# Kernel tuning notes

Hardware: AMD Instinct MI355X
Metric: run time of the kernel (lower is better)

Reference implementation:

```python
import jax, jax.numpy as jnp
import numpy as np

N, K, C, OUT = 2048, 14, 512, 512
SCALE = 4.0
BN_EPS = 1e-5


def _edge_lists(k):
    # pairs i<j with i,j != k-1 and adj[i,j] > 0 (adj is fully connected ones)
    ei, ej = [], []
    for i in range(k - 1):
        for j in range(i + 1, k - 1):
            ei.append(i)
            ej.append(j)
    return np.asarray(ei, np.int32), np.asarray(ej, np.int32)


def setup_inputs() -> dict:
    key = jax.random.key(0)
    k0, k1, k2, k3 = jax.random.split(key, 4)
    ei, ej = _edge_lists(K)
    std = 0.02
    return {
        "inputs": jax.random.normal(k0, (N, K, C), dtype=jnp.float32),
        "adj": jnp.ones((K, K), dtype=jnp.float32),
        "edge_i": jnp.asarray(ei),
        "edge_j": jnp.asarray(ej),
        "gamma": jnp.ones((C,), dtype=jnp.float32),
        "beta": jnp.zeros((C,), dtype=jnp.float32),
        "w_direct": jax.random.normal(k1, (C,), dtype=jnp.float32) * std,
        "W_merged": jax.random.normal(k2, (OUT, C), dtype=jnp.float32) * std,
        "W_orig": jax.random.normal(k3, (OUT, C), dtype=jnp.float32) * std,
    }


def reference(inputs, adj, edge_i, edge_j, gamma, beta, w_direct, W_merged, W_orig):
    n, k, c = inputs.shape
    # --- learn_adj ---
    global_feat = inputs[:, k - 1 : k, :]                      # [N,1,c]
    distances = jnp.abs(inputs - global_feat)                  # [N,k,c]
    # pairwise gaps only on the static edge list (i<j, non-global, adj>0)
    gap = 15.0 * (distances[:, edge_i, :] - distances[:, edge_j, :])  # [N,E,c]
    # BatchNorm1d over channel c, batch stats over (N, E), biased variance
    mean = jnp.mean(gap, axis=(0, 1))
    var = jnp.mean(jnp.square(gap - mean), axis=(0, 1))
    bn = (gap - mean) * (gamma / jnp.sqrt(var + BN_EPS)) + beta        # [N,E,c]
    a = jax.nn.sigmoid(SCALE * jnp.einsum("nec,c->ne", bn, w_direct))  # [N,E]
    adj2 = jnp.ones((n, k, k), dtype=inputs.dtype)
    adj2 = adj2.at[:, edge_i, edge_j].set(2.0 * a)
    adj2 = adj2.at[:, edge_j, edge_i].set(2.0 * (1.0 - a))
    new_adj = adj2 * adj[None, :, :]
    norm = jnp.sum(jnp.abs(new_adj), axis=2, keepdims=True)    # L1 row norm
    new_adj = new_adj / jnp.maximum(norm, 1e-12)
    # --- graph conv ---
    agg = jnp.einsum("nij,njc->nic", new_adj, inputs)          # [N,k,c]
    merged = jax.nn.relu(jnp.einsum("nkc,oc->nko", agg, W_merged))
    original = jnp.einsum("nkc,oc->nko", inputs, W_orig)
    return merged + original
```

## Files before the change

kernel.cpp:

```cpp
#include <hip/hip_runtime.h>
#include <stdint.h>

#define K_NODES 14
#define C_DIM   512
#define OUT_DIM 512
#define N_EDGE  78

typedef float  f32x4  __attribute__((ext_vector_type(4)));
typedef __bf16 bf16x8 __attribute__((ext_vector_type(8)));

__device__ __forceinline__ unsigned short f2bf(float f) {
    unsigned int u = __builtin_bit_cast(unsigned int, f);
    unsigned int r = (u + 0x7fffu + ((u >> 16) & 1u)) >> 16;
    return (unsigned short)r;
}
__device__ __forceinline__ float bf2f(unsigned short s) {
    return __builtin_bit_cast(float, (unsigned int)s << 16);
}

__device__ __forceinline__ void async16(const void* g, void* l) {
    __builtin_amdgcn_global_load_lds(
        (const __attribute__((address_space(1))) unsigned int*)g,
        (__attribute__((address_space(3))) unsigned int*)l, 16, 0, 0);
}

__global__ __launch_bounds__(1024) void stats_partial(
    const float* __restrict__ x, float* __restrict__ part,
    unsigned short* __restrict__ xbf,
    const float* __restrict__ Wm, const float* __restrict__ Wo,
    unsigned short* __restrict__ wmbf, unsigned short* __restrict__ wobf)
{
    int t  = threadIdx.x;
    int q  = t & 127;
    int sn = t >> 7;
    int n  = blockIdx.x * 8 + sn;
    size_t base = (size_t)n * K_NODES * C_DIM + q * 4;

    f32x4 g = *(const f32x4*)(x + base + 13 * C_DIM);
    ushort4 gb; gb.x=f2bf(g.x); gb.y=f2bf(g.y); gb.z=f2bf(g.z); gb.w=f2bf(g.w);
    *(ushort4*)(xbf + base + 13 * C_DIM) = gb;

    float S10=0,S11=0,S12=0,S13=0, S20=0,S21=0,S22=0,S23=0, Sw0=0,Sw1=0,Sw2=0,Sw3=0;
    #pragma unroll
    for (int k = 0; k < 13; ++k) {
        f32x4 v = *(const f32x4*)(x + base + k * C_DIM);
        ushort4 vb; vb.x=f2bf(v.x); vb.y=f2bf(v.y); vb.z=f2bf(v.z); vb.w=f2bf(v.w);
        *(ushort4*)(xbf + base + k * C_DIM) = vb;
        float wk = (float)(12 - 2 * k);
        float d0=fabsf(v.x-g.x), d1=fabsf(v.y-g.y), d2=fabsf(v.z-g.z), d3=fabsf(v.w-g.w);
        S10+=d0; S11+=d1; S12+=d2; S13+=d3;
        S20+=d0*d0; S21+=d1*d1; S22+=d2*d2; S23+=d3*d3;
        Sw0+=wk*d0; Sw1+=wk*d1; Sw2+=wk*d2; Sw3+=wk*d3;
    }
    f32x4 as = (f32x4){15.f*Sw0, 15.f*Sw1, 15.f*Sw2, 15.f*Sw3};
    f32x4 aq = (f32x4){225.f*(13.f*S20 - S10*S10), 225.f*(13.f*S21 - S11*S11),
                       225.f*(13.f*S22 - S12*S12), 225.f*(13.f*S23 - S13*S13)};

    __shared__ f32x4 redS[8][128];
    __shared__ f32x4 redQ[8][128];
    redS[sn][q] = as;
    redQ[sn][q] = aq;
    __syncthreads();
    if (sn == 0) {
        f32x4 s = redS[0][q], z = redQ[0][q];
        #pragma unroll
        for (int r = 1; r < 8; ++r) { s += redS[r][q]; z += redQ[r][q]; }
        *(f32x4*)(part + (size_t)blockIdx.x * 1024 + q * 4)       = s;
        *(f32x4*)(part + (size_t)blockIdx.x * 1024 + 512 + q * 4) = z;
    }
    int i0 = blockIdx.x * 1024 + t;
    wmbf[i0] = f2bf(Wm[i0]);
    wobf[i0] = f2bf(Wo[i0]);
}

__global__ __launch_bounds__(256) void finalize_stats(
    const float* __restrict__ part, float inv_ne,
    const float* __restrict__ gamma, const float* __restrict__ beta,
    const float* __restrict__ wdir, float* __restrict__ u, float* __restrict__ bpart)
{
    int lane = threadIdx.x & 63;
    int wv   = threadIdx.x >> 6;
    int c    = blockIdx.x * 64 + lane;
    float s = 0.f, q = 0.f;
    #pragma unroll 8
    for (int r = wv; r < 256; r += 4) {
        s += part[(size_t)r * 1024 + c];
        q += part[(size_t)r * 1024 + 512 + c];
    }
    __shared__ float shs[4][64], shq[4][64];
    shs[wv][lane] = s; shq[wv][lane] = q;
    __syncthreads();
    if (wv == 0) {
        s = shs[0][lane] + shs[1][lane] + shs[2][lane] + shs[3][lane];
        q = shq[0][lane] + shq[1][lane] + shq[2][lane] + shq[3][lane];
        float mean = s * inv_ne;
        float var  = q * inv_ne - mean * mean;
        float sc   = gamma[c] / sqrtf(var + 1e-5f);
        u[c] = sc * wdir[c];
        float b = (beta[c] - mean * sc) * wdir[c];
        #pragma unroll
        for (int off = 1; off < 64; off <<= 1) b += __shfl_xor(b, off, 64);
        if (lane == 0) bpart[blockIdx.x] = b;
    }
}

__global__ __launch_bounds__(256) void fuse_graph(
    const unsigned short* __restrict__ xbf, const float* __restrict__ adj,
    const int* __restrict__ ei, const int* __restrict__ ej,
    const float* __restrict__ u, const float* __restrict__ bpart,
    unsigned short* __restrict__ aggbf)
{
    __shared__ float WL[2][196];
    __shared__ float Dp[2][2][13];
    __shared__ float invL[2][14];
    int wv = threadIdx.x >> 6, lane = threadIdx.x & 63;
    int sp = wv >> 1;
    int h  = wv & 1;
    int n  = blockIdx.x * 2 + sp;
    size_t base = (size_t)n * K_NODES * C_DIM + h * 256 + lane * 4;

    float xf[K_NODES][4];
    #pragma unroll
    for (int k = 0; k < K_NODES; ++k) {
        uint2 raw = *(const uint2*)(xbf + base + k * C_DIM);
        xf[k][0]=bf2f(raw.x&0xffff); xf[k][1]=bf2f(raw.x>>16);
        xf[k][2]=bf2f(raw.y&0xffff); xf[k][3]=bf2f(raw.y>>16);
    }
    f32x4 uv = *(const f32x4*)(u + h * 256 + lane * 4);

    #pragma unroll
    for (int k = 0; k < 13; ++k) {
        float p = fabsf(xf[k][0]-xf[13][0])*uv.x + fabsf(xf[k][1]-xf[13][1])*uv.y
                + fabsf(xf[k][2]-xf[13][2])*uv.z + fabsf(xf[k][3]-xf[13][3])*uv.w;
        #pragma unroll
        for (int off = 1; off < 64; off <<= 1) p += __shfl_xor(p, off, 64);
        if (lane == 0) Dp[sp][h][k] = p;
    }
    __syncthreads();

    if (h == 0) {
        float bc = 0.f;
        #pragma unroll
        for (int b8 = 0; b8 < 8; ++b8) bc += bpart[b8];
        for (int e = lane; e < N_EDGE; e += 64) {
            int ii = ei[e], jj = ej[e];
            float Di = Dp[sp][0][ii] + Dp[sp][1][ii];
            float Dj = Dp[sp][0][jj] + Dp[sp][1][jj];
            float z = 4.0f * (15.f * (Di - Dj) + bc);
            float a = 1.f / (1.f + expf(-z));
            WL[sp][ii * K_NODES + jj] = adj[ii * K_NODES + jj] * (2.f * a);
            WL[sp][jj * K_NODES + ii] = adj[jj * K_NODES + ii] * (2.f * (1.f - a));
        }
    } else {
        for (int idx = lane; idx < K_NODES * K_NODES; idx += 64) {
            int i = idx / K_NODES, j = idx - i * K_NODES;
            if (i == j || i == 13 || j == 13) WL[sp][idx] = adj[idx];
        }
    }
    __syncthreads();
    if (h == 0 && lane < K_NODES) {
        float s = 0.f;
        #pragma unroll
        for (int j = 0; j < K_NODES; ++j) s += fabsf(WL[sp][lane * K_NODES + j]);
        invL[sp][lane] = 1.f / fmaxf(s, 1e-12f);
    }
    __syncthreads();

    #pragma unroll
    for (int i = 0; i < K_NODES; ++i) {
        float s0=0.f,s1=0.f,s2=0.f,s3=0.f;
        #pragma unroll
        for (int j = 0; j < K_NODES; ++j) {
            float w = WL[sp][i * K_NODES + j];
            s0 += w*xf[j][0]; s1 += w*xf[j][1]; s2 += w*xf[j][2]; s3 += w*xf[j][3];
        }
        float wi = invL[sp][i];
        uint2 r;
        r.x = (unsigned int)f2bf(s0*wi) | ((unsigned int)f2bf(s1*wi) << 16);
        r.y = (unsigned int)f2bf(s2*wi) | ((unsigned int)f2bf(s3*wi) << 16);
        *(uint2*)(aggbf + base + i * C_DIM) = r;
    }
}

#define TM 128
#define TN 128
#define BK 32

__global__ __launch_bounds__(256, 3) void gemm_fused(
    const unsigned short* __restrict__ Aagg, const unsigned short* __restrict__ Axin,
    const unsigned short* __restrict__ Bwm,  const unsigned short* __restrict__ Bwo,
    float* __restrict__ out)
{
    __shared__ unsigned short lA[3][TM * BK];
    __shared__ unsigned short lB[3][TN * BK];
    int tid  = threadIdx.x;
    int lane = tid & 63;
    int wave = tid >> 6;
    int wr = wave >> 1, wc = wave & 1;
    int bm = blockIdx.x * TM;
    int bn = blockIdx.y * TN;

    f32x4 acc[4][4];
    #pragma unroll
    for (int i = 0; i < 4; ++i)
        #pragma unroll
        for (int j = 0; j < 4; ++j) acc[i][j] = (f32x4){0.f, 0.f, 0.f, 0.f};

    int lrow = lane & 15;
    int kc   = lane >> 4;
    int pcs  = (kc ^ ((lrow >> 1) & 3)) * 8;
    int srow = lane >> 2;
    int scol = lane & 3;
    int lc   = scol ^ ((srow >> 1) & 3);
    size_t goff0 = (size_t)(wave * 16 + srow) * C_DIM + lc * 8;
    size_t goff1 = goff0 + (size_t)64 * C_DIM;

#define STAGE(buf, Ap, Bp, kb)                                               \
    {                                                                         \
        async16((Ap) + (size_t)bm * C_DIM + (kb) + goff0,                     \
                &lA[buf][(wave * 16) * BK]);                                  \
        async16((Ap) + (size_t)bm * C_DIM + (kb) + goff1,                     \
                &lA[buf][(64 + wave * 16) * BK]);                             \
        async16((Bp) + (size_t)bn * C_DIM + (kb) + goff0,                     \
                &lB[buf][(wave * 16) * BK]);                                  \
        async16((Bp) + (size_t)bn * C_DIM + (kb) + goff1,                     \
                &lB[buf][(64 + wave * 16) * BK]);                             \
    }

    STAGE(0, Aagg, Bwm, 0);
    STAGE(1, Aagg, Bwm, BK);
    asm volatile("s_waitcnt vmcnt(4)" ::: "memory");
    __builtin_amdgcn_s_barrier();

    #pragma unroll 32
    for (int t = 0; t < 32; ++t) {
        if (t + 2 < 32) {
            const unsigned short* Ap = ((t + 2) < 16) ? Aagg : Axin;
            const unsigned short* Bp = ((t + 2) < 16) ? Bwm  : Bwo;
            STAGE((t + 2) % 3, Ap, Bp, ((t + 2) & 15) * BK);
        }
        {
            const int buf = t % 3;
            bf16x8 af[4], bfr[4];
            #pragma unroll
            for (int i = 0; i < 4; ++i)
                af[i] = *(const bf16x8*)&lA[buf][(wr * 64 + i * 16 + lrow) * BK + pcs];
            #pragma unroll
            for (int j = 0; j < 4; ++j)
                bfr[j] = *(const bf16x8*)&lB[buf][(wc * 64 + j * 16 + lrow) * BK + pcs];
            __builtin_amdgcn_s_setprio(1);
            #pragma unroll
            for (int i = 0; i < 4; ++i)
                #pragma unroll
                for (int j = 0; j < 4; ++j)
                    acc[i][j] = __builtin_amdgcn_mfma_f32_16x16x32_bf16(
                        af[i], bfr[j], acc[i][j], 0, 0, 0);
            __builtin_amdgcn_s_setprio(0);
        }
        if (t == 15) {
            #pragma unroll
            for (int i = 0; i < 4; ++i)
                #pragma unroll
                for (int j = 0; j < 4; ++j)
                    #pragma unroll
                    for (int r = 0; r < 4; ++r)
                        acc[i][j][r] = fmaxf(acc[i][j][r], 0.f);
        }
        asm volatile("s_waitcnt lgkmcnt(0)" ::: "memory");
        __builtin_amdgcn_sched_barrier(0);
        if (t < 30)      asm volatile("s_waitcnt vmcnt(4)" ::: "memory");
        else             asm volatile("s_waitcnt vmcnt(0)" ::: "memory");
        if (t < 31) __builtin_amdgcn_s_barrier();
    }
#undef STAGE

    int orow0 = bm + wr * 64 + (lane >> 4) * 4;
    int ocol0 = bn + wc * 64 + (lane & 15);
    #pragma unroll
    for (int i = 0; i < 4; ++i)
        #pragma unroll
        for (int j = 0; j < 4; ++j)
            #pragma unroll
            for (int r = 0; r < 4; ++r)
                out[(size_t)(orow0 + i * 16 + r) * OUT_DIM + (ocol0 + j * 16)] = acc[i][j][r];
}

extern "C" void kernel_launch(void* const* d_in, const int* in_sizes, int n_in,
                              void* d_out, int out_size, void* d_ws, size_t ws_size,
                              hipStream_t stream)
{
    const float* x     = (const float*)d_in[0];
    const float* adj   = (const float*)d_in[1];
    const int*   ei    = (const int*)d_in[2];
    const int*   ej    = (const int*)d_in[3];
    const float* gamma = (const float*)d_in[4];
    const float* beta  = (const float*)d_in[5];
    const float* wdir  = (const float*)d_in[6];
    const float* Wm    = (const float*)d_in[7];
    const float* Wo    = (const float*)d_in[8];
    float* out = (float*)d_out;

    int N = in_sizes[0] / (K_NODES * C_DIM);
    int M = N * K_NODES;

    float* ws_f   = (float*)d_ws;
    float* u      = ws_f + 1024;
    float* bpart  = ws_f + 1536;
    float* part   = ws_f + 2048;
    char*  wsb    = (char*)d_ws;
    size_t off    = (size_t)(2048 + 256 * 1024) * sizeof(float);
    unsigned short* wmbf  = (unsigned short*)(wsb + off);  off += (size_t)OUT_DIM * C_DIM * 2;
    unsigned short* wobf  = (unsigned short*)(wsb + off);  off += (size_t)OUT_DIM * C_DIM * 2;
    unsigned short* xbf   = (unsigned short*)(wsb + off);  off += (size_t)M * C_DIM * 2;
    unsigned short* aggbf = (unsigned short*)(wsb + off);

    float inv_ne = 1.0f / ((float)N * (float)N_EDGE);

    hipLaunchKernelGGL(stats_partial, dim3(N / 8), dim3(1024), 0, stream,
                       x, part, xbf, Wm, Wo, wmbf, wobf);
    hipLaunchKernelGGL(finalize_stats, dim3(8), dim3(256), 0, stream,
                       part, inv_ne, gamma, beta, wdir, u, bpart);
    hipLaunchKernelGGL(fuse_graph, dim3(N / 2), dim3(256), 0, stream,
                       xbf, adj, ei, ej, u, bpart, aggbf);
    hipLaunchKernelGGL(gemm_fused, dim3(M / TM, OUT_DIM / TN), dim3(256), 0, stream,
                       aggbf, xbf, wmbf, wobf, out);
}
```

Measured before the change: 185.5 us.

## Enlarge GEMM tile to 256x128 with BK=64 and 8 waves per block

Grows the fused GEMM block tile from 128x128 to 256x128 with 512 threads (8 waves, each still computing a 64x64 sub-tile), and doubles the K step to 64. The loop now runs 16 iterations, each doing two MFMA sub-steps. Staging loads and the LDS XOR swizzle are reworked for the wider K rows. The aim is more operand reuse per loaded byte and half as many barriers per K. In exchange it uses more LDS per block, launches fewer blocks (M/256 x 4) and so risks lower occupancy and a coarser tail.

```diff
diff --git a/kernel.cpp b/kernel.cpp
--- a/kernel.cpp
+++ b/kernel.cpp
@@ -182,11 +182,11 @@
     }
 }
 
-#define TM 128
+#define TM 256
 #define TN 128
-#define BK 32
-
-__global__ __launch_bounds__(256, 3) void gemm_fused(
+#define BK 64
+
+__global__ __launch_bounds__(512, 2) void gemm_fused(
     const unsigned short* __restrict__ Aagg, const unsigned short* __restrict__ Axin,
     const unsigned short* __restrict__ Bwm,  const unsigned short* __restrict__ Bwo,
     float* __restrict__ out)
@@ -196,7 +196,8 @@
     int tid  = threadIdx.x;
     int lane = tid & 63;
     int wave = tid >> 6;
-    int wr = wave >> 1, wc = wave & 1;
+    int wr = wave >> 1;
+    int wc = wave & 1;
     int bm = blockIdx.x * TM;
     int bn = blockIdx.y * TN;
 
@@ -207,57 +208,57 @@
         for (int j = 0; j < 4; ++j) acc[i][j] = (f32x4){0.f, 0.f, 0.f, 0.f};
 
     int lrow = lane & 15;
-    int kc   = lane >> 4;
-    int pcs  = (kc ^ ((lrow >> 1) & 3)) * 8;
-    int srow = lane >> 2;
-    int scol = lane & 3;
-    int lc   = scol ^ ((srow >> 1) & 3);
-    size_t goff0 = (size_t)(wave * 16 + srow) * C_DIM + lc * 8;
-    size_t goff1 = goff0 + (size_t)64 * C_DIM;
+    int xorv = lane & 7;
+    int srow = tid >> 3;
+    int lcu  = ((tid & 7) ^ (srow & 7)) * 8;
 
 #define STAGE(buf, Ap, Bp, kb)                                               \
     {                                                                         \
-        async16((Ap) + (size_t)bm * C_DIM + (kb) + goff0,                     \
-                &lA[buf][(wave * 16) * BK]);                                  \
-        async16((Ap) + (size_t)bm * C_DIM + (kb) + goff1,                     \
-                &lA[buf][(64 + wave * 16) * BK]);                             \
-        async16((Bp) + (size_t)bn * C_DIM + (kb) + goff0,                     \
-                &lB[buf][(wave * 16) * BK]);                                  \
-        async16((Bp) + (size_t)bn * C_DIM + (kb) + goff1,                     \
-                &lB[buf][(64 + wave * 16) * BK]);                             \
+        _Pragma("unroll")                                                     \
+        for (int it = 0; it < 4; ++it)                                        \
+            async16((Ap) + (size_t)(bm + it * 64 + srow) * C_DIM + (kb) + lcu,\
+                    &lA[buf][(it * 64 + wave * 8) * BK]);                     \
+        _Pragma("unroll")                                                     \
+        for (int it = 0; it < 2; ++it)                                        \
+            async16((Bp) + (size_t)(bn + it * 64 + srow) * C_DIM + (kb) + lcu,\
+                    &lB[buf][(it * 64 + wave * 8) * BK]);                     \
     }
 
     STAGE(0, Aagg, Bwm, 0);
     STAGE(1, Aagg, Bwm, BK);
-    asm volatile("s_waitcnt vmcnt(4)" ::: "memory");
+    asm volatile("s_waitcnt vmcnt(6)" ::: "memory");
     __builtin_amdgcn_s_barrier();
 
-    #pragma unroll 32
-    for (int t = 0; t < 32; ++t) {
-        if (t + 2 < 32) {
-            const unsigned short* Ap = ((t + 2) < 16) ? Aagg : Axin;
-            const unsigned short* Bp = ((t + 2) < 16) ? Bwm  : Bwo;
-            STAGE((t + 2) % 3, Ap, Bp, ((t + 2) & 15) * BK);
+    #pragma unroll
+    for (int t = 0; t < 16; ++t) {
+        if (t + 2 < 16) {
+            const unsigned short* Ap = ((t + 2) < 8) ? Aagg : Axin;
+            const unsigned short* Bp = ((t + 2) < 8) ? Bwm  : Bwo;
+            STAGE((t + 2) % 3, Ap, Bp, ((t + 2) & 7) * BK);
         }
         {
             const int buf = t % 3;
-            bf16x8 af[4], bfr[4];
             #pragma unroll
-            for (int i = 0; i < 4; ++i)
-                af[i] = *(const bf16x8*)&lA[buf][(wr * 64 + i * 16 + lrow) * BK + pcs];
-            #pragma unroll
-            for (int j = 0; j < 4; ++j)
-                bfr[j] = *(const bf16x8*)&lB[buf][(wc * 64 + j * 16 + lrow) * BK + pcs];
-            __builtin_amdgcn_s_setprio(1);
-            #pragma unroll
-            for (int i = 0; i < 4; ++i)
+            for (int ks = 0; ks < 2; ++ks) {
+                int pcs = ((ks * 4 + (lane >> 4)) ^ xorv) * 8;
+                bf16x8 af[4], bfr[4];
+                #pragma unroll
+                for (int i = 0; i < 4; ++i)
+                    af[i] = *(const bf16x8*)&lA[buf][(wr * 64 + i * 16 + lrow) * BK + pcs];
                 #pragma unroll
                 for (int j = 0; j < 4; ++j)
-                    acc[i][j] = __builtin_amdgcn_mfma_f32_16x16x32_bf16(
-                        af[i], bfr[j], acc[i][j], 0, 0, 0);
-            __builtin_amdgcn_s_setprio(0);
-        }
-        if (t == 15) {
+                    bfr[j] = *(const bf16x8*)&lB[buf][(wc * 64 + j * 16 + lrow) * BK + pcs];
+                __builtin_amdgcn_s_setprio(1);
+                #pragma unroll
+                for (int i = 0; i < 4; ++i)
+                    #pragma unroll
+                    for (int j = 0; j < 4; ++j)
+                        acc[i][j] = __builtin_amdgcn_mfma_f32_16x16x32_bf16(
+                            af[i], bfr[j], acc[i][j], 0, 0, 0);
+                __builtin_amdgcn_s_setprio(0);
+            }
+        }
+        if (t == 7) {
             #pragma unroll
             for (int i = 0; i < 4; ++i)
                 #pragma unroll
@@ -268,9 +269,9 @@
         }
         asm volatile("s_waitcnt lgkmcnt(0)" ::: "memory");
         __builtin_amdgcn_sched_barrier(0);
-        if (t < 30)      asm volatile("s_waitcnt vmcnt(4)" ::: "memory");
-        else             asm volatile("s_waitcnt vmcnt(0)" ::: "memory");
-        if (t < 31) __builtin_amdgcn_s_barrier();
+        if (t < 14)      asm volatile("s_waitcnt vmcnt(6)" ::: "memory");
+        else if (t == 14) asm volatile("s_waitcnt vmcnt(0)" ::: "memory");
+        if (t < 15) __builtin_amdgcn_s_barrier();
     }
 #undef STAGE
 
@@ -322,6 +323,6 @@
                        part, inv_ne, gamma, beta, wdir, u, bpart);
     hipLaunchKernelGGL(fuse_graph, dim3(N / 2), dim3(256), 0, stream,
                        xbf, adj, ei, ej, u, bpart, aggbf);
-    hipLaunchKernelGGL(gemm_fused, dim3(M / TM, OUT_DIM / TN), dim3(256), 0, stream,
+    hipLaunchKernelGGL(gemm_fused, dim3(M / TM, OUT_DIM / TN), dim3(512), 0, stream,
                        aggbf, xbf, wmbf, wobf, out);
 }
```

Result: no change. 184.0 us (-0.8%).
